# Performance work log

Measured on AMD Instinct MI355X. Metric: run time of the kernel, lower is better.

The kernel has to match this reference:

```python
import jax, jax.numpy as jnp
import numpy as np

FEAT_STRIDE = 16
PRE_NMS = 6000
POST_NMS = 300
NMS_THRESH = 0.7


def _whctrs(a):
    w = a[2] - a[0] + 1.0
    h = a[3] - a[1] + 1.0
    return w, h, a[0] + 0.5 * (w - 1), a[1] + 0.5 * (h - 1)

def _mkanchors(ws, hs, xc, yc):
    return np.stack([xc - 0.5 * (ws - 1), yc - 0.5 * (hs - 1),
                     xc + 0.5 * (ws - 1), yc + 0.5 * (hs - 1)], axis=1)

def _ratio_enum(anchor, ratios):
    w, h, xc, yc = _whctrs(anchor)
    size = w * h
    ws = np.round(np.sqrt(size / ratios))
    hs = np.round(ws * ratios)
    return _mkanchors(ws, hs, xc, yc)

def _scale_enum(anchor, scales):
    w, h, xc, yc = _whctrs(anchor)
    return _mkanchors(w * scales, h * scales, xc, yc)

def generate_anchors(base_size=16, ratios=np.array([0.5, 1.0, 2.0]), scales=np.array([8, 16, 32])):
    base = np.array([1, 1, base_size, base_size], dtype=np.float64) - 1
    ra = _ratio_enum(base, np.asarray(ratios, np.float64))
    return np.vstack([_scale_enum(ra[i], np.asarray(scales, np.float64)) for i in range(ra.shape[0])])


def setup_inputs() -> dict:
    key = jax.random.key(0)
    k1, k2 = jax.random.split(key)
    B, A, H, W = 8, 9, 64, 64
    scores = jax.random.normal(k1, (B, 2 * A, H, W), jnp.float32)
    bbox_deltas = jax.random.normal(k2, (B, 4 * A, H, W), jnp.float32)
    anchors = jnp.asarray(generate_anchors(16), jnp.float32)  # [9, 4]
    return {"scores": scores, "bbox_deltas": bbox_deltas, "anchors": anchors,
            "image_width": 1024, "image_height": 1024}


def _nms_keep(iou, thresh):
    # greedy NMS on score-sorted boxes given a full IoU matrix
    n = iou.shape[0]
    idx = jnp.arange(n)
    def body(i, keep):
        sup = keep[i] & (iou[i] > thresh) & (idx > i)
        return keep & ~sup
    return jax.lax.fori_loop(0, n, body, jnp.ones((n,), bool))


def _nms_one(boxes):  # boxes [PRE_NMS, 4], sorted by score desc
    b = jax.lax.stop_gradient(boxes)
    area = (b[:, 2] - b[:, 0] + 1.0) * (b[:, 3] - b[:, 1] + 1.0)
    iw = jnp.clip(jnp.minimum(b[:, None, 2], b[None, :, 2]) -
                  jnp.maximum(b[:, None, 0], b[None, :, 0]) + 1.0, 0.0)
    ih = jnp.clip(jnp.minimum(b[:, None, 3], b[None, :, 3]) -
                  jnp.maximum(b[:, None, 1], b[None, :, 1]) + 1.0, 0.0)
    inter = iw * ih
    iou = inter / (area[:, None] + area[None, :] - inter)
    keep = _nms_keep(iou, NMS_THRESH)
    # compact kept boxes to the front, pad with zeros (fixed shape)
    rank = jnp.cumsum(keep) - 1
    dest = jnp.where(keep, rank, PRE_NMS)  # suppressed -> dump row
    out = jnp.zeros((PRE_NMS + 1, 4), boxes.dtype).at[dest].set(boxes)
    return out[:POST_NMS]


def _forward(scores, bbox_deltas, anchors, image_width, image_height):
    B = scores.shape[0]
    A = anchors.shape[0]
    H, W = scores.shape[2], scores.shape[3]
    fg = scores[:, A:, :, :]                                   # [B, A, H, W]
    # shifted anchor grid
    mx, my = jnp.meshgrid(jnp.arange(W) * FEAT_STRIDE, jnp.arange(H) * FEAT_STRIDE)
    shifts = jnp.stack([mx.ravel(), my.ravel(), mx.ravel(), my.ravel()], 1).astype(scores.dtype)
    all_anchors = (shifts[:, None, :] + anchors[None, :, :]).reshape(-1, 4)  # [K*A, 4]
    deltas = bbox_deltas.transpose(0, 2, 3, 1).reshape(B, -1, 4)             # [B, K*A, 4]
    sc = fg.transpose(0, 2, 3, 1).reshape(B, -1)                             # [B, K*A]
    # bbox_transform_inv
    aw = all_anchors[:, 2] - all_anchors[:, 0] + 1.0
    ah = all_anchors[:, 3] - all_anchors[:, 1] + 1.0
    acx = all_anchors[:, 0] + 0.5 * aw
    acy = all_anchors[:, 1] + 0.5 * ah
    pcx = deltas[..., 0] * aw + acx
    pcy = deltas[..., 1] * ah + acy
    pw = jnp.exp(deltas[..., 2]) * aw
    ph = jnp.exp(deltas[..., 3]) * ah
    # clip to image
    x1 = jnp.clip(pcx - 0.5 * pw, 0.0, image_width - 1)
    y1 = jnp.clip(pcy - 0.5 * ph, 0.0, image_height - 1)
    x2 = jnp.clip(pcx + 0.5 * pw, 0.0, image_width - 1)
    y2 = jnp.clip(pcy + 0.5 * ph, 0.0, image_height - 1)
    proposals = jnp.stack([x1, y1, x2, y2], -1)                 # [B, K*A, 4]
    # per-image pre-NMS top-k by score
    _, order = jax.lax.top_k(sc, PRE_NMS)
    boxes = jnp.take_along_axis(proposals, order[..., None], axis=1)  # [B, PRE, 4]
    props = jax.lax.map(_nms_one, boxes)                        # [B, POST, 4]
    bidx = jnp.broadcast_to(jnp.arange(B, dtype=props.dtype)[:, None, None], (B, POST_NMS, 1))
    return jnp.concatenate([bidx, props], axis=-1)              # [B, POST, 5]


def reference(scores, bbox_deltas, anchors, image_width, image_height):
    return _forward(scores, bbox_deltas, anchors, image_width, image_height)
```

## Files before the change

### kernel.cpp

```cpp
#include <hip/hip_runtime.h>
#include <math.h>

#pragma clang fp contract(off)

#define BB 8
#define AA 9
#define NPIX 4096
#define NN (NPIX*AA)
#define PRE 6000
#define POST 300
#define SELCAP 7000
#define TMAX 10111
#define HZW 5120

#define RA 0x3F000000u
#define RB 0x41000000u
__device__ __forceinline__ unsigned key_bin2(unsigned k) {
    return (k < RA) ? (k >> 17) : (8064u + ((k - RA) >> 14));
}

#define SMEM_BYTES 65536

__device__ __forceinline__ unsigned score_key(float s) {
    unsigned fb = __float_as_uint(s);
    unsigned u = (fb & 0x80000000u) ? ~fb : (fb | 0x80000000u);
    return ~u;
}

__device__ __forceinline__ unsigned phalf(unsigned v, unsigned bin) {
    return (v >> ((bin & 1) << 4)) & 0xFFFFu;
}

__device__ __forceinline__ bool iou_gt(float ax1, float ay1, float ax2, float ay2, float aa,
                                       float bx1_, float by1_, float bx2_, float by2_, float ab) {
    float xx1 = fmaxf(ax1, bx1_);
    float yy1 = fmaxf(ay1, by1_);
    float xx2 = fminf(ax2, bx2_);
    float yy2 = fminf(ay2, by2_);
    float iw = fmaxf(xx2 - xx1 + 1.0f, 0.0f);
    float ih = fmaxf(yy2 - yy1 + 1.0f, 0.0f);
    float inter = iw * ih;
    float uni = (aa + ab) - inter;
    return (double)inter >= 0x1.666667p-1 * (double)uni;
}

__device__ __forceinline__ void dec_issue(int g, const unsigned short* sorted16,
                                          const float* anch, const float* deltas_b,
                                          float* aw, float* ah, float* acx, float* acy,
                                          float* d0, float* d1, float* d2, float* d3) {
    unsigned idx = sorted16[(g < PRE) ? g : (PRE - 1)];
    int a = (int)(idx % AA);
    int pix = (int)(idx / AA);
    int wq = pix & 63, hq = pix >> 6;
    float sx = (float)(wq * 16), sy = (float)(hq * 16);
    float ax1 = anch[a * 4 + 0] + sx, ay1 = anch[a * 4 + 1] + sy;
    float ax2 = anch[a * 4 + 2] + sx, ay2 = anch[a * 4 + 3] + sy;
    float w_ = ax2 - ax1 + 1.0f, h_ = ay2 - ay1 + 1.0f;
    *aw = w_; *ah = h_;
    *acx = ax1 + 0.5f * w_; *acy = ay1 + 0.5f * h_;
    const float* dp = deltas_b + (size_t)(a * 4) * NPIX + pix;
    *d0 = dp[0]; *d1 = dp[NPIX]; *d2 = dp[2 * NPIX]; *d3 = dp[3 * NPIX];
}

__device__ __forceinline__ void dec_finish(float aw, float ah, float acx, float acy,
                                           float d0, float d1, float d2, float d3,
                                           float fw, float fh, float4* bx, float* ar) {
    float pcx = d0 * aw + acx, pcy = d1 * ah + acy;
    float pw = expf(d2) * aw, ph = expf(d3) * ah;
    float x1 = fminf(fmaxf(pcx - 0.5f * pw, 0.0f), fw);
    float y1 = fminf(fmaxf(pcy - 0.5f * ph, 0.0f), fh);
    float x2 = fminf(fmaxf(pcx + 0.5f * pw, 0.0f), fw);
    float y2 = fminf(fmaxf(pcy + 0.5f * ph, 0.0f), fh);
    *bx = make_float4(x1, y1, x2, y2);
    *ar = (x2 - x1 + 1.0f) * (y2 - y1 + 1.0f);
}

__device__ __forceinline__ void decode_box(int g, const unsigned short* sorted16,
                                           const float* anch, const float* deltas_b,
                                           float fw, float fh, float4* bx, float* ar) {
    float aw, ah, acx, acy, d0, d1, d2, d3;
    dec_issue(g, sorted16, anch, deltas_b, &aw, &ah, &acx, &acy, &d0, &d1, &d2, &d3);
    dec_finish(aw, ah, acx, acy, d0, d1, d2, d3, fw, fh, bx, ar);
}

__device__ __forceinline__ void bar_lds() {
    asm volatile("s_waitcnt lgkmcnt(0)" ::: "memory");
    __builtin_amdgcn_s_barrier();
    asm volatile("" ::: "memory");
}

__global__ __launch_bounds__(1024) void proposal_kernel(const float* __restrict__ scores,
                                                        const float* __restrict__ deltas,
                                                        const float* __restrict__ anchors,
                                                        const int* __restrict__ imw,
                                                        const int* __restrict__ imh,
                                                        float* __restrict__ out) {
    __shared__ __align__(16) unsigned char smem[SMEM_BYTES];
    unsigned*       hist32 = (unsigned*)smem;
    unsigned*       keyh   = (unsigned*)(smem + 20480);
    unsigned short* idxl   = (unsigned short*)(smem + 48512);
    unsigned*       scal   = (unsigned*)(smem + 65344);
    unsigned short* sorted16 = (unsigned short*)(smem + 20480);
    float4*         kb4  = (float4*)smem;
    float*          kba  = (float*)(smem + 4800);
    float4*         cnd4 = (float4*)(smem + 6016);
    float*          cnda = (float*)(smem + 8064);
    unsigned long long* srow  = (unsigned long long*)(smem + 8576);
    unsigned char*  dead8 = (unsigned char*)(smem + 9600);
    float*          anch = (float*)(smem + 9856);

    int b = blockIdx.x;
    int tid = threadIdx.x;
    int wave = tid >> 6, lane = tid & 63;
    const float* sc = scores + (size_t)(b * (2 * AA) + AA) * NPIX;
    const float4* sc4 = (const float4*)sc;
    const float* deltas_b = deltas + (size_t)b * (4 * AA) * NPIX;
    float fw = (float)(imw[0] - 1);
    float fh = (float)(imh[0] - 1);

    for (int j = tid; j < HZW; j += 1024) hist32[j] = 0;
    __syncthreads();
    #pragma unroll
    for (int q = 0; q < 9; ++q) {
        float4 v = sc4[(q << 10) + tid];
        unsigned k0 = score_key(v.x), k1 = score_key(v.y);
        unsigned k2 = score_key(v.z), k3 = score_key(v.w);
        if (k0 < RB) { unsigned b0 = key_bin2(k0); atomicAdd(&hist32[b0 >> 1], 1u << ((b0 & 1) << 4)); }
        if (k1 < RB) { unsigned b1 = key_bin2(k1); atomicAdd(&hist32[b1 >> 1], 1u << ((b1 & 1) << 4)); }
        if (k2 < RB) { unsigned b2 = key_bin2(k2); atomicAdd(&hist32[b2 >> 1], 1u << ((b2 & 1) << 4)); }
        if (k3 < RB) { unsigned b3 = key_bin2(k3); atomicAdd(&hist32[b3 >> 1], 1u << ((b3 & 1) << 4)); }
    }
    __syncthreads();

    unsigned ssum = 0;
    const unsigned* hw = hist32 + tid * 16;
    if (tid < 320) {
        #pragma unroll
        for (int j = 0; j < 16; ++j) { unsigned w = hw[j]; ssum += (w & 0xFFFFu) + (w >> 16); }
    }
    unsigned x = ssum;
    #pragma unroll
    for (int d = 1; d < 64; d <<= 1) {
        unsigned y = __shfl_up(x, (unsigned)d, 64);
        if (lane >= d) x += y;
    }
    if (lane == 63 && wave < 5) scal[wave] = x;
    __syncthreads();
    unsigned wexcl = 0;
    #pragma unroll
    for (int w = 0; w < 5; ++w) if (w < wave) wexcl += scal[w];
    unsigned gexcl = wexcl + (x - ssum);
    unsigned gincl = gexcl + ssum;
    if (tid == 319) { scal[16] = TMAX; scal[17] = gincl; }
    __syncthreads();
    if (tid < 320 && gexcl <= (PRE - 1) && (PRE - 1) < gincl) {
        unsigned c = gexcl, T = tid * 32, tot = gincl;
        bool f = false;
        for (int j = 0; j < 32 && !f; ++j) {
            unsigned d = phalf(hw[j >> 1], (unsigned)j);
            if ((PRE - 1) < c + d) { T = tid * 32 + j; tot = c + d; f = true; }
            c += d;
        }
        scal[16] = T;
        scal[17] = tot;
    }
    __syncthreads();
    unsigned T = scal[16];
    if (T > TMAX) T = TMAX;
    unsigned cnt = scal[17];
    if (cnt > SELCAP) cnt = SELCAP;

    if ((unsigned)(tid * 32) <= T) {
        unsigned run = gexcl;
        unsigned* wv = hist32 + tid * 16;
        #pragma unroll
        for (int j = 0; j < 16; ++j) {
            unsigned v = wv[j];
            unsigned c0 = v & 0xFFFFu, c1 = v >> 16;
            wv[j] = run | ((run + c0) << 16);
            run += c0 + c1;
        }
    }
    __syncthreads();

    #pragma unroll
    for (int q = 0; q < 9; ++q) {
        float4 v = sc4[(q << 10) + tid];
        #pragma unroll
        for (int c = 0; c < 4; ++c) {
            float s = (c == 0) ? v.x : (c == 1) ? v.y : (c == 2) ? v.z : v.w;
            unsigned k = score_key(s);
            if (k < RB) {
                unsigned bin = key_bin2(k);
                if (bin <= T) {
                    unsigned old = atomicAdd(&hist32[bin >> 1], 1u << ((bin & 1) << 4));
                    unsigned pos = phalf(old, bin);
                    if (pos < SELCAP) {
                        keyh[pos] = k;
                        int pix = (tid << 2) + c;
                        idxl[pos] = (unsigned short)(pix * AA + q);
                    }
                }
            }
        }
    }
    __syncthreads();

    unsigned rnk8[8], id8[8];
    #pragma unroll
    for (int m = 0; m < 8; ++m) {
        int s = (m << 10) + tid;
        rnk8[m] = 0xFFFFFFFFu;
        if (s < (int)cnt) {
            unsigned k = keyh[s];
            unsigned id = idxl[s];
            unsigned bin = key_bin2(k);
            unsigned start = bin ? phalf(hist32[(bin - 1) >> 1], bin - 1) : 0u;
            unsigned end = phalf(hist32[bin >> 1], bin);
            if (end > cnt) end = cnt;
            if (start > end) start = end;
            unsigned rank = start;
            for (unsigned j = start; j < end; ++j) {
                unsigned kj = keyh[j];
                rank += (kj < k) ? 1u : 0u;
                if (kj == k) rank += ((unsigned)idxl[j] < id) ? 1u : 0u;
            }
            rnk8[m] = rank;
            id8[m] = id;
        }
    }
    __syncthreads();
    #pragma unroll
    for (int m = 0; m < 8; ++m)
        if (rnk8[m] < PRE) sorted16[rnk8[m]] = (unsigned short)id8[m];
    if (tid < 36) anch[tid] = anchors[tid];
    __syncthreads();

    float s_aw = 0.f, s_ah = 0.f, s_acx = 0.f, s_acy = 0.f;
    float s_d0 = 0.f, s_d1 = 0.f, s_d2 = 0.f, s_d3 = 0.f;

    if (tid < 64) {
        float4 bx; float ar;
        decode_box(tid, sorted16, anch, deltas_b, fw, fh, &bx, &ar);
        cnd4[tid] = bx; cnda[tid] = ar;
    }
    if (wave == 8)
        dec_issue(64 + lane, sorted16, anch, deltas_b,
                  &s_aw, &s_ah, &s_acx, &s_acy, &s_d0, &s_d1, &s_d2, &s_d3);
    __syncthreads();

    int w15 = (wave < 8) ? wave : (wave - 1);
    int nc = (w15 < 4) ? 5 : 4;
    int cstart = (w15 < 4) ? (w15 * 5) : (20 + (w15 - 4) * 4);
    int c4off = (nc == 5) ? 4 : 3;

    int cur = 0, K = 0, p = 0, pb = 0;
    for (;;) {
        float4 mc = cnd4[p * 64 + lane];
        float ma = cnda[p * 64 + lane];
        float4 cj0 = cnd4[p * 64 + wave];
        float4 cj1 = cnd4[p * 64 + 16 + wave];
        float4 cj2 = cnd4[p * 64 + 32 + wave];
        float4 cj3 = cnd4[p * 64 + 48 + wave];
        float aj0 = cnda[p * 64 + wave];
        float aj1 = cnda[p * 64 + 16 + wave];
        float aj2 = cnda[p * 64 + 32 + wave];
        float aj3 = cnda[p * 64 + 48 + wave];

        if (wave == 8) {
            float4 nb; float na;
            dec_finish(s_aw, s_ah, s_acx, s_acy, s_d0, s_d1, s_d2, s_d3,
                       fw, fh, &nb, &na);
            cnd4[(p ^ 1) * 64 + lane] = nb;
            cnda[(p ^ 1) * 64 + lane] = na;
            dec_issue(cur + 128 + lane, sorted16, anch, deltas_b,
                      &s_aw, &s_ah, &s_acx, &s_acy, &s_d0, &s_d1, &s_d2, &s_d3);
        }

        float4 cb0, cb1, cb2, cb3, cb4;
        float  ab0, ab1, ab2, ab3, ab4;
        float4 kv; float ka;
        if (wave != 8) {
            cb0 = cnd4[p * 64 + cstart + 0];  ab0 = cnda[p * 64 + cstart + 0];
            cb1 = cnd4[p * 64 + cstart + 1];  ab1 = cnda[p * 64 + cstart + 1];
            cb2 = cnd4[p * 64 + cstart + 2];  ab2 = cnda[p * 64 + cstart + 2];
            cb3 = cnd4[p * 64 + cstart + 3];  ab3 = cnda[p * 64 + cstart + 3];
            cb4 = cnd4[p * 64 + cstart + c4off]; ab4 = cnda[p * 64 + cstart + c4off];
            int k0 = (lane < K) ? lane : 0;
            kv = kb4[k0]; ka = kba[k0];
        }

        {
            int j = wave;
            bool g = (lane < j) && iou_gt(mc.x, mc.y, mc.z, mc.w, ma,
                                          cj0.x, cj0.y, cj0.z, cj0.w, aj0);
            unsigned long long bl = __ballot(g);
            if (lane == 0) srow[pb * 64 + j] = bl;
        }
        {
            int j = 16 + wave;
            bool g = (lane < j) && iou_gt(mc.x, mc.y, mc.z, mc.w, ma,
                                          cj1.x, cj1.y, cj1.z, cj1.w, aj1);
            unsigned long long bl = __ballot(g);
            if (lane == 0) srow[pb * 64 + j] = bl;
        }
        {
            int j = 32 + wave;
            bool g = (lane < j) && iou_gt(mc.x, mc.y, mc.z, mc.w, ma,
                                          cj2.x, cj2.y, cj2.z, cj2.w, aj2);
            unsigned long long bl = __ballot(g);
            if (lane == 0) srow[pb * 64 + j] = bl;
        }
        {
            int j = 48 + wave;
            bool g = (lane < j) && iou_gt(mc.x, mc.y, mc.z, mc.w, ma,
                                          cj3.x, cj3.y, cj3.z, cj3.w, aj3);
            unsigned long long bl = __ballot(g);
            if (lane == 0) srow[pb * 64 + j] = bl;
        }

        if (wave != 8) {
            bool dd0 = (cur + cstart + 0 >= PRE);
            bool dd1 = (cur + cstart + 1 >= PRE);
            bool dd2 = (cur + cstart + 2 >= PRE);
            bool dd3 = (cur + cstart + 3 >= PRE);
            bool dd4 = (cur + cstart + 4 >= PRE);
            unsigned todo = 0;
            if (!dd0) todo |= 1u;
            if (!dd1) todo |= 2u;
            if (!dd2) todo |= 4u;
            if (!dd3) todo |= 8u;
            if (nc == 5 && !dd4) todo |= 16u;
            for (int t = 0; (t << 6) < K && todo; ++t) {
                int kn = ((t + 1) << 6) + lane;
                int knn = (kn < K) ? kn : 0;
                float4 kvn = kb4[knn]; float kan = kba[knn];
                bool kval = ((t << 6) + lane) < K;
                if (todo & 1u) {
                    bool hit = kval && iou_gt(kv.x, kv.y, kv.z, kv.w, ka,
                                              cb0.x, cb0.y, cb0.z, cb0.w, ab0);
                    if (__ballot(hit) != 0ULL) { dd0 = true; todo &= ~1u; }
                }
                if (todo & 2u) {
                    bool hit = kval && iou_gt(kv.x, kv.y, kv.z, kv.w, ka,
                                              cb1.x, cb1.y, cb1.z, cb1.w, ab1);
                    if (__ballot(hit) != 0ULL) { dd1 = true; todo &= ~2u; }
                }
                if (todo & 4u) {
                    bool hit = kval && iou_gt(kv.x, kv.y, kv.z, kv.w, ka,
                                              cb2.x, cb2.y, cb2.z, cb2.w, ab2);
                    if (__ballot(hit) != 0ULL) { dd2 = true; todo &= ~4u; }
                }
                if (todo & 8u) {
                    bool hit = kval && iou_gt(kv.x, kv.y, kv.z, kv.w, ka,
                                              cb3.x, cb3.y, cb3.z, cb3.w, ab3);
                    if (__ballot(hit) != 0ULL) { dd3 = true; todo &= ~8u; }
                }
                if (todo & 16u) {
                    bool hit = kval && iou_gt(kv.x, kv.y, kv.z, kv.w, ka,
                                              cb4.x, cb4.y, cb4.z, cb4.w, ab4);
                    if (__ballot(hit) != 0ULL) { dd4 = true; todo &= ~16u; }
                }
                kv = kvn; ka = kan;
            }
            if (lane == 0) {
                dead8[pb * 64 + cstart + 0] = dd0 ? 1 : 0;
                dead8[pb * 64 + cstart + 1] = dd1 ? 1 : 0;
                dead8[pb * 64 + cstart + 2] = dd2 ? 1 : 0;
                dead8[pb * 64 + cstart + 3] = dd3 ? 1 : 0;
                if (nc == 5) dead8[pb * 64 + cstart + 4] = dd4 ? 1 : 0;
            }
        }

        bar_lds();

        bool dead = dead8[pb * 64 + lane] != 0;
        unsigned long long dk = __ballot(dead);
        unsigned long long row = srow[pb * 64 + lane];
        unsigned long long live = ~dk;
        unsigned long long keptb = 0ULL;
        int allowed = POST - K;
        while (live) {
            int f = __ffsll((long long)live) - 1;
            keptb |= (1ULL << f);
            if (__popcll(keptb) >= allowed) break;
            bool die = (row >> f) & 1ULL;
            unsigned long long dbl = __ballot(die);
            live &= ~(dbl | (1ULL << f));
        }
        int nkeep = __popcll(keptb);
        int take = (nkeep < allowed) ? nkeep : allowed;

        if ((keptb >> lane) & 1ULL) {
            int rnk = __popcll(keptb & ((1ULL << lane) - 1ULL));
            if (rnk < take) { kb4[K + rnk] = mc; kba[K + rnk] = ma; }
        }
        K += take;
        cur += 64;
        if (K >= POST || cur >= PRE) break;
        p ^= 1; pb ^= 1;
    }

    __syncthreads();
    for (int idx = tid; idx < POST * 5; idx += 1024) {
        int row_ = idx / 5;
        int col = idx - row_ * 5;
        float val = 0.0f;
        if (row_ < K) {
            float4 v = kb4[row_];
            val = (col == 0) ? (float)b : (col == 1) ? v.x : (col == 2) ? v.y
                : (col == 3) ? v.z : v.w;
        }
        out[(size_t)b * POST * 5 + idx] = val;
    }
}

extern "C" void kernel_launch(void* const* d_in, const int* in_sizes, int n_in,
                              void* d_out, int out_size, void* d_ws, size_t ws_size,
                              hipStream_t stream) {
    const float* scores  = (const float*)d_in[0];
    const float* deltas  = (const float*)d_in[1];
    const float* anchors = (const float*)d_in[2];
    const int*   imw     = (const int*)d_in[3];
    const int*   imh     = (const int*)d_in[4];
    float* out = (float*)d_out;

    proposal_kernel<<<BB, 1024, 0, stream>>>(scores, deltas, anchors, imw, imh, out);
}
```

Baseline: 149.6 us.

## Compute in-chunk suppression lazily via shuffles and add float IoU fast path

Removes the precomputed 64x64 intra-chunk suppression matrix (srow) that every wave built each iteration. The serial greedy scan now broadcasts each newly kept box with shuffles and evaluates IoU against the chunk on the fly. The IoU test is also rewritten to use a float fma with an error band, falling back to the double-precision comparison only for borderline cases, which avoids double math in the common case. The trade-off is more serial work inside the per-chunk keep loop, executed redundantly by every wave.

```diff
diff --git a/kernel.cpp b/kernel.cpp
--- a/kernel.cpp
+++ b/kernel.cpp
@@ -41,7 +41,12 @@
     float ih = fmaxf(yy2 - yy1 + 1.0f, 0.0f);
     float inter = iw * ih;
     float uni = (aa + ab) - inter;
-    return (double)inter >= 0x1.666667p-1 * (double)uni;
+    float d = fmaf(-0.7f, uni, inter);
+    bool res  = d >= uni * 0x1.08p-20f;
+    bool bord = !res && (d >= uni * -0x1.fp-21f);
+    if (bord)
+        res = ((double)inter >= 0x1.666667p-1 * (double)uni);
+    return res;
 }
 
 __device__ __forceinline__ void dec_issue(int g, const unsigned short* sorted16,
@@ -105,7 +110,6 @@
     float*          kba  = (float*)(smem + 4800);
     float4*         cnd4 = (float4*)(smem + 6016);
     float*          cnda = (float*)(smem + 8064);
-    unsigned long long* srow  = (unsigned long long*)(smem + 8576);
     unsigned char*  dead8 = (unsigned char*)(smem + 9600);
     float*          anch = (float*)(smem + 9856);
 
@@ -258,14 +262,6 @@
     for (;;) {
         float4 mc = cnd4[p * 64 + lane];
         float ma = cnda[p * 64 + lane];
-        float4 cj0 = cnd4[p * 64 + wave];
-        float4 cj1 = cnd4[p * 64 + 16 + wave];
-        float4 cj2 = cnd4[p * 64 + 32 + wave];
-        float4 cj3 = cnd4[p * 64 + 48 + wave];
-        float aj0 = cnda[p * 64 + wave];
-        float aj1 = cnda[p * 64 + 16 + wave];
-        float aj2 = cnda[p * 64 + 32 + wave];
-        float aj3 = cnda[p * 64 + 48 + wave];
 
         if (wave == 8) {
             float4 nb; float na;
@@ -277,49 +273,15 @@
                       &s_aw, &s_ah, &s_acx, &s_acy, &s_d0, &s_d1, &s_d2, &s_d3);
         }
 
-        float4 cb0, cb1, cb2, cb3, cb4;
-        float  ab0, ab1, ab2, ab3, ab4;
-        float4 kv; float ka;
         if (wave != 8) {
-            cb0 = cnd4[p * 64 + cstart + 0];  ab0 = cnda[p * 64 + cstart + 0];
-            cb1 = cnd4[p * 64 + cstart + 1];  ab1 = cnda[p * 64 + cstart + 1];
-            cb2 = cnd4[p * 64 + cstart + 2];  ab2 = cnda[p * 64 + cstart + 2];
-            cb3 = cnd4[p * 64 + cstart + 3];  ab3 = cnda[p * 64 + cstart + 3];
-            cb4 = cnd4[p * 64 + cstart + c4off]; ab4 = cnda[p * 64 + cstart + c4off];
+            float4 cb0 = cnd4[p * 64 + cstart + 0];  float ab0 = cnda[p * 64 + cstart + 0];
+            float4 cb1 = cnd4[p * 64 + cstart + 1];  float ab1 = cnda[p * 64 + cstart + 1];
+            float4 cb2 = cnd4[p * 64 + cstart + 2];  float ab2 = cnda[p * 64 + cstart + 2];
+            float4 cb3 = cnd4[p * 64 + cstart + 3];  float ab3 = cnda[p * 64 + cstart + 3];
+            float4 cb4 = cnd4[p * 64 + cstart + c4off]; float ab4 = cnda[p * 64 + cstart + c4off];
             int k0 = (lane < K) ? lane : 0;
-            kv = kb4[k0]; ka = kba[k0];
-        }
-
-        {
-            int j = wave;
-            bool g = (lane < j) && iou_gt(mc.x, mc.y, mc.z, mc.w, ma,
-                                          cj0.x, cj0.y, cj0.z, cj0.w, aj0);
-            unsigned long long bl = __ballot(g);
-            if (lane == 0) srow[pb * 64 + j] = bl;
-        }
-        {
-            int j = 16 + wave;
-            bool g = (lane < j) && iou_gt(mc.x, mc.y, mc.z, mc.w, ma,
-                                          cj1.x, cj1.y, cj1.z, cj1.w, aj1);
-            unsigned long long bl = __ballot(g);
-            if (lane == 0) srow[pb * 64 + j] = bl;
-        }
-        {
-            int j = 32 + wave;
-            bool g = (lane < j) && iou_gt(mc.x, mc.y, mc.z, mc.w, ma,
-                                          cj2.x, cj2.y, cj2.z, cj2.w, aj2);
-            unsigned long long bl = __ballot(g);
-            if (lane == 0) srow[pb * 64 + j] = bl;
-        }
-        {
-            int j = 48 + wave;
-            bool g = (lane < j) && iou_gt(mc.x, mc.y, mc.z, mc.w, ma,
-                                          cj3.x, cj3.y, cj3.z, cj3.w, aj3);
-            unsigned long long bl = __ballot(g);
-            if (lane == 0) srow[pb * 64 + j] = bl;
-        }
-
-        if (wave != 8) {
+            float4 kv = kb4[k0]; float ka = kba[k0];
+
             bool dd0 = (cur + cstart + 0 >= PRE);
             bool dd1 = (cur + cstart + 1 >= PRE);
             bool dd2 = (cur + cstart + 2 >= PRE);
@@ -376,7 +338,6 @@
 
         bool dead = dead8[pb * 64 + lane] != 0;
         unsigned long long dk = __ballot(dead);
-        unsigned long long row = srow[pb * 64 + lane];
         unsigned long long live = ~dk;
         unsigned long long keptb = 0ULL;
         int allowed = POST - K;
@@ -384,7 +345,13 @@
             int f = __ffsll((long long)live) - 1;
             keptb |= (1ULL << f);
             if (__popcll(keptb) >= allowed) break;
-            bool die = (row >> f) & 1ULL;
+            float fx1 = __shfl(mc.x, f);
+            float fy1 = __shfl(mc.y, f);
+            float fx2 = __shfl(mc.z, f);
+            float fy2 = __shfl(mc.w, f);
+            float fa  = __shfl(ma, f);
+            bool die = (lane > f) && iou_gt(fx1, fy1, fx2, fy2, fa,
+                                            mc.x, mc.y, mc.z, mc.w, ma);
             unsigned long long dbl = __ballot(die);
             live &= ~(dbl | (1ULL << f));
         }
```

Measured after the change: 190.0 us. +27.0%, slower.
